# Kernel tuning notes

Measured on AMD Instinct MI355X. Metric: run time of the kernel, lower is better.

The kernel has to match this reference:

```python
import jax, jax.numpy as jnp
import numpy as np

D_MODEL = 1024
NUM_HEADS = 16
D_K = D_MODEL // NUM_HEADS


def setup_inputs() -> dict:
    key = jax.random.key(0)
    ks = jax.random.split(key, 8)
    B, S = 2, 2048
    query = jax.random.normal(ks[0], (B, S, D_MODEL), dtype=jnp.float32)
    k_in = jax.random.normal(ks[1], (B, S, D_MODEL), dtype=jnp.float32)
    value = jax.random.normal(ks[2], (B, S, D_MODEL), dtype=jnp.float32)
    # causal mask: True = masked out (upper triangle above diagonal)
    mask = jnp.triu(jnp.ones((S, S), dtype=bool), k=1)[None, None, :, :]
    scale = 1.0 / np.sqrt(D_MODEL)
    W_q = jax.random.normal(ks[3], (D_MODEL, D_MODEL), dtype=jnp.float32) * scale
    W_k = jax.random.normal(ks[4], (D_MODEL, D_MODEL), dtype=jnp.float32) * scale
    W_v = jax.random.normal(ks[5], (D_MODEL, D_MODEL), dtype=jnp.float32) * scale
    W_o = jax.random.normal(ks[6], (D_MODEL, D_MODEL), dtype=jnp.float32) * scale
    return {"query": query, "key": k_in, "value": value, "mask": mask,
            "W_q": W_q, "W_k": W_k, "W_v": W_v, "W_o": W_o}


def _split(x):
    # [B, S, d_model] -> [B, h, S, d_k]
    B, S, _ = x.shape
    return x.reshape(B, S, NUM_HEADS, D_K).transpose(0, 2, 1, 3)


def reference(query, key, value, mask, W_q, W_k, W_v, W_o):
    # torch nn.Linear(bias=False): y = x @ W.T
    Q = _split(query @ W_q.T)   # [B, h, Sq, d_k]
    K = _split(key @ W_k.T)     # [B, h, Sk, d_k]
    V = _split(value @ W_v.T)   # [B, h, Sk, d_k]
    scores = jnp.einsum('bhqd,bhkd->bhqk', Q, K) / jnp.sqrt(jnp.float32(D_K))
    scores = jnp.where(mask, -jnp.inf, scores)
    attn_w = jax.nn.softmax(scores, axis=-1)
    attn_w = jnp.nan_to_num(attn_w, nan=0.0)
    out = jnp.einsum('bhqk,bhkd->bhqd', attn_w, V)  # [B, h, Sq, d_k]
    B, _, Sq, _ = out.shape
    merged = out.transpose(0, 2, 1, 3).reshape(B, Sq, D_MODEL)
    return merged @ W_o.T
```

## Files before the change

kernel.cpp:

```cpp
#include <hip/hip_runtime.h>
#include <hip/hip_bf16.h>
#include <stdint.h>

typedef __attribute__((ext_vector_type(4))) float f32x4;
typedef __attribute__((ext_vector_type(8))) __bf16 bf16x8;
typedef __attribute__((ext_vector_type(4))) unsigned short us4;

#define SEQ 2048
#define DMODEL 1024
#define NH 16
#define DK 64
#define MTOT 4096

__device__ __forceinline__ unsigned short f2bf(float x) {
  union { float f; unsigned int u; } v; v.f = x;
  unsigned int r = v.u + 0x7fffu + ((v.u >> 16) & 1u);
  return (unsigned short)(r >> 16);
}

__device__ __forceinline__ unsigned int cvtpk(float lo, float hi) {
  unsigned int r;
  asm("v_cvt_pk_bf16_f32 %0, %1, %2" : "=v"(r) : "v"(lo), "v"(hi));
  return r;
}

__device__ __forceinline__ f32x4 mfma_bf16(bf16x8 a, bf16x8 b, f32x4 c) {
  return __builtin_amdgcn_mfma_f32_16x16x32_bf16(a, b, c, 0, 0, 0);
}

__device__ __forceinline__ void gload16(const unsigned short* g, unsigned short* l) {
  __builtin_amdgcn_global_load_lds((__attribute__((address_space(1))) void*)g,
                                   (__attribute__((address_space(3))) void*)l,
                                   16, 0, 0);
}

__global__ void cvt_all(const float* __restrict__ s0, const float* __restrict__ s1,
                        const float* __restrict__ s2, const float* __restrict__ s3,
                        const float* __restrict__ s4, const float* __restrict__ s5,
                        const float* __restrict__ s6,
                        unsigned short* __restrict__ d0, unsigned short* __restrict__ d1,
                        unsigned short* __restrict__ d2, unsigned short* __restrict__ d3,
                        unsigned short* __restrict__ d4, unsigned short* __restrict__ d5,
                        unsigned short* __restrict__ d6) {
  const int y = blockIdx.y;
  const float* s = y == 0 ? s0 : y == 1 ? s1 : y == 2 ? s2 : y == 3 ? s3
                 : y == 4 ? s4 : y == 5 ? s5 : s6;
  unsigned short* d = y == 0 ? d0 : y == 1 ? d1 : y == 2 ? d2 : y == 3 ? d3
                    : y == 4 ? d4 : y == 5 ? d5 : d6;
  const int n4 = (y < 3) ? (MTOT * DMODEL / 4) : (DMODEL * DMODEL / 4);
  const int stride = gridDim.x * blockDim.x;
  for (int i = blockIdx.x * blockDim.x + threadIdx.x; i < n4; i += stride) {
    f32x4 v = reinterpret_cast<const f32x4*>(s)[i];
    us4 o;
    o.x = f2bf(v.x); o.y = f2bf(v.y); o.z = f2bf(v.z); o.w = f2bf(v.w);
    reinterpret_cast<us4*>(d)[i] = o;
  }
}

__global__ __launch_bounds__(256) void gemm_qkv(
    const unsigned short* __restrict__ xq, const unsigned short* __restrict__ xk,
    const unsigned short* __restrict__ xv, const unsigned short* __restrict__ bwq,
    const unsigned short* __restrict__ bwk, const unsigned short* __restrict__ bwv,
    unsigned short* __restrict__ Qh, unsigned short* __restrict__ Kh,
    unsigned short* __restrict__ Vt) {
  const int z = blockIdx.z;
  const unsigned short* A = z == 0 ? xq : (z == 1 ? xk : xv);
  const unsigned short* B = z == 0 ? bwq : (z == 1 ? bwk : bwv);
  unsigned short* out = z == 0 ? Qh : (z == 1 ? Kh : Vt);
  const float scale = z == 0 ? 0.18033688011112042f : 1.0f;

  __shared__ __align__(16) unsigned short lA[128 * 32];
  __shared__ __align__(16) unsigned short lB[128 * 32];
  const int tid = threadIdx.x;
  const int lane = tid & 63;
  const int wid = tid >> 6;
  const int l15 = lane & 15, l4 = lane >> 4;
  const int bm = blockIdx.x, bn = blockIdx.y;
  const int wr = wid >> 1, wc = wid & 1;

  f32x4 acc[4][4] = {};

  const int chunk0 = (wid * 2 + 0) * 64 + lane;
  const int chunk1 = (wid * 2 + 1) * 64 + lane;
  const unsigned short* gA0 = A + (size_t)(bm * 128 + (chunk0 >> 2)) * 1024 + (chunk0 & 3) * 8;
  const unsigned short* gA1 = A + (size_t)(bm * 128 + (chunk1 >> 2)) * 1024 + (chunk1 & 3) * 8;
  const unsigned short* gB0 = B + (size_t)(bn * 128 + (chunk0 >> 2)) * 1024 + (chunk0 & 3) * 8;
  const unsigned short* gB1 = B + (size_t)(bn * 128 + (chunk1 >> 2)) * 1024 + (chunk1 & 3) * 8;
  unsigned short* lA0 = lA + (wid * 2 + 0) * 512;
  unsigned short* lA1 = lA + (wid * 2 + 1) * 512;
  unsigned short* lB0 = lB + (wid * 2 + 0) * 512;
  unsigned short* lB1 = lB + (wid * 2 + 1) * 512;

  for (int kt = 0; kt < 1024; kt += 32) {
    __syncthreads();
    gload16(gA0 + kt, lA0);
    gload16(gA1 + kt, lA1);
    gload16(gB0 + kt, lB0);
    gload16(gB1 + kt, lB1);
    __syncthreads();
    bf16x8 af[4], bfr[4];
#pragma unroll
    for (int i = 0; i < 4; ++i)
      af[i] = *reinterpret_cast<const bf16x8*>(&lA[(wr * 64 + i * 16 + l15) * 32 + l4 * 8]);
#pragma unroll
    for (int j = 0; j < 4; ++j)
      bfr[j] = *reinterpret_cast<const bf16x8*>(&lB[(wc * 64 + j * 16 + l15) * 32 + l4 * 8]);
#pragma unroll
    for (int i = 0; i < 4; ++i)
#pragma unroll
      for (int j = 0; j < 4; ++j)
        acc[i][j] = mfma_bf16(af[i], bfr[j], acc[i][j]);
  }

  const int row0 = bm * 128 + wr * 64;
  const int col0 = bn * 128 + wc * 64;

  if (z < 2) {
#pragma unroll
    for (int i = 0; i < 4; ++i) {
#pragma unroll
      for (int j = 0; j < 4; ++j) {
        const int n = col0 + j * 16 + l15;
        const int h = n >> 6, dd = n & 63;
#pragma unroll
        for (int r = 0; r < 4; ++r) {
          const int m = row0 + i * 16 + l4 * 4 + r;
          const int b = m >> 11, s = m & 2047;
          out[(size_t)(b * NH + h) * (SEQ * DK) + s * DK + dd] = f2bf(acc[i][j][r] * scale);
        }
      }
    }
  } else {
#pragma unroll
    for (int i = 0; i < 4; ++i) {
      const int m0 = row0 + i * 16 + l4 * 4;
      const int b = m0 >> 11, s0 = m0 & 2047;
      const int g = (s0 >> 2) & 7;
      const int col = (s0 & ~31) + ((g & 3) << 3) + ((g >> 2) << 2);
#pragma unroll
      for (int j = 0; j < 4; ++j) {
        const int n = col0 + j * 16 + l15;
        const int h = n >> 6, dd = n & 63;
        us4 pk;
        pk.x = f2bf(acc[i][j][0]);
        pk.y = f2bf(acc[i][j][1]);
        pk.z = f2bf(acc[i][j][2]);
        pk.w = f2bf(acc[i][j][3]);
        *reinterpret_cast<us4*>(&out[(size_t)(b * NH + h) * (DK * SEQ) + dd * SEQ + col]) = pk;
      }
    }
  }
}

__global__ __launch_bounds__(256) void gemm_o(const unsigned short* __restrict__ A,
                                              const unsigned short* __restrict__ B,
                                              float* __restrict__ out) {
  __shared__ __align__(16) unsigned short lA[128 * 32];
  __shared__ __align__(16) unsigned short lB[128 * 32];
  const int tid = threadIdx.x;
  const int lane = tid & 63;
  const int wid = tid >> 6;
  const int l15 = lane & 15, l4 = lane >> 4;
  const int bm = blockIdx.x, bn = blockIdx.y;
  const int wr = wid >> 1, wc = wid & 1;

  f32x4 acc[4][4] = {};

  const int chunk0 = (wid * 2 + 0) * 64 + lane;
  const int chunk1 = (wid * 2 + 1) * 64 + lane;
  const unsigned short* gA0 = A + (size_t)(bm * 128 + (chunk0 >> 2)) * 1024 + (chunk0 & 3) * 8;
  const unsigned short* gA1 = A + (size_t)(bm * 128 + (chunk1 >> 2)) * 1024 + (chunk1 & 3) * 8;
  const unsigned short* gB0 = B + (size_t)(bn * 128 + (chunk0 >> 2)) * 1024 + (chunk0 & 3) * 8;
  const unsigned short* gB1 = B + (size_t)(bn * 128 + (chunk1 >> 2)) * 1024 + (chunk1 & 3) * 8;
  unsigned short* lA0 = lA + (wid * 2 + 0) * 512;
  unsigned short* lA1 = lA + (wid * 2 + 1) * 512;
  unsigned short* lB0 = lB + (wid * 2 + 0) * 512;
  unsigned short* lB1 = lB + (wid * 2 + 1) * 512;

  for (int kt = 0; kt < 1024; kt += 32) {
    __syncthreads();
    gload16(gA0 + kt, lA0);
    gload16(gA1 + kt, lA1);
    gload16(gB0 + kt, lB0);
    gload16(gB1 + kt, lB1);
    __syncthreads();
    bf16x8 af[4], bfr[4];
#pragma unroll
    for (int i = 0; i < 4; ++i)
      af[i] = *reinterpret_cast<const bf16x8*>(&lA[(wr * 64 + i * 16 + l15) * 32 + l4 * 8]);
#pragma unroll
    for (int j = 0; j < 4; ++j)
      bfr[j] = *reinterpret_cast<const bf16x8*>(&lB[(wc * 64 + j * 16 + l15) * 32 + l4 * 8]);
#pragma unroll
    for (int i = 0; i < 4; ++i)
#pragma unroll
      for (int j = 0; j < 4; ++j)
        acc[i][j] = mfma_bf16(af[i], bfr[j], acc[i][j]);
  }

  const int row0 = bm * 128 + wr * 64;
  const int col0 = bn * 128 + wc * 64;
#pragma unroll
  for (int i = 0; i < 4; ++i)
#pragma unroll
    for (int j = 0; j < 4; ++j)
#pragma unroll
      for (int r = 0; r < 4; ++r) {
        const int m = row0 + i * 16 + l4 * 4 + r;
        const int n = col0 + j * 16 + l15;
        out[(size_t)m * DMODEL + n] = acc[i][j][r];
      }
}

__global__ __launch_bounds__(512, 2) void attn_kernel(const unsigned short* __restrict__ Qh,
                                                      const unsigned short* __restrict__ Kh,
                                                      const unsigned short* __restrict__ Vt,
                                                      unsigned short* __restrict__ Mg) {
  __shared__ __align__(16) unsigned short Kl[3][64 * 64];
  __shared__ __align__(16) unsigned short Vl[3][64 * 64];

  const int tid = threadIdx.x;
  const int lane = tid & 63;
  const int w = tid >> 6;
  const int l15 = lane & 15, l4 = lane >> 4;

  const int d = blockIdx.x;
  const int xcd = d & 7;
  const int j = d >> 3;
  const int bh = (j >> 3) * 8 + xcd;
  const int x = j & 7;

  const unsigned short* Qb = Qh + (size_t)bh * SEQ * DK;
  const unsigned short* Kb = Kh + (size_t)bh * SEQ * DK;
  const unsigned short* Vb = Vt + (size_t)bh * DK * SEQ;
  const int bq = bh >> 4, hh = bh & 15;
  unsigned short* Mbase = Mg + (size_t)bq * SEQ * DMODEL + hh * DK;

  const int srow = lane >> 3;
  const int sswz = (lane & 7) ^ srow;
  const unsigned short* KsrcB = Kb + (size_t)(w * 8 + srow) * DK + sswz * 8;
  const unsigned short* VsrcB = Vb + (size_t)(w * 8 + srow) * SEQ + sswz * 8;

  const int l7 = l15 & 7;

  const int taus[2] = {15 - x, x};

#pragma unroll 1
  for (int seg = 0; seg < 2; ++seg) {
    const int tau = taus[seg];
    const int qbase = tau * 128;
    const int q0w = qbase + w * 16;
    const int nt = 2 * tau + 2;

    __syncthreads();

    bf16x8 qf0 = *reinterpret_cast<const bf16x8*>(Qb + (size_t)(q0w + l15) * DK + l4 * 8);
    bf16x8 qf1 = *reinterpret_cast<const bf16x8*>(Qb + (size_t)(q0w + l15) * DK + 32 + l4 * 8);

    f32x4 o[4] = {};
    float mrow = -__builtin_inff();
    float lrow = 0.0f;

    gload16(KsrcB, &Kl[0][w * 512]);
    gload16(VsrcB, &Vl[0][w * 512]);
    gload16(KsrcB + (size_t)64 * DK, &Kl[1][w * 512]);
    gload16(VsrcB + 64, &Vl[1][w * 512]);

    int bi = 0;
#pragma unroll 1
    for (int t = 0; t < nt; ++t) {
      const int kbase = t << 6;
      if (t + 1 < nt) {
        asm volatile("s_waitcnt vmcnt(2)" ::: "memory");
      } else {
        asm volatile("s_waitcnt vmcnt(0)" ::: "memory");
      }
      __builtin_amdgcn_sched_barrier(0);
      __builtin_amdgcn_s_barrier();
      __builtin_amdgcn_sched_barrier(0);

      if (t + 2 < nt) {
        const int pb = (bi == 0) ? 2 : bi - 1;
        gload16(KsrcB + (size_t)(kbase + 128) * DK, &Kl[pb][w * 512]);
        gload16(VsrcB + (kbase + 128), &Vl[pb][w * 512]);
      }

      if (kbase < q0w + 16) {
        const unsigned short* Kc = Kl[bi];
        const unsigned short* Vc = Vl[bi];

        f32x4 sc[4];
        __builtin_amdgcn_s_setprio(1);
#pragma unroll
        for (int c = 0; c < 4; ++c) {
          const int krow = c * 16 + l15;
          bf16x8 kf0 = *reinterpret_cast<const bf16x8*>(&Kc[krow * 64 + ((l4 ^ l7) * 8)]);
          bf16x8 kf1 = *reinterpret_cast<const bf16x8*>(&Kc[krow * 64 + (((4 + l4) ^ l7) * 8)]);
          f32x4 z = {0.f, 0.f, 0.f, 0.f};
          z = mfma_bf16(kf0, qf0, z);
          sc[c] = mfma_bf16(kf1, qf1, z);
        }
        __builtin_amdgcn_s_setprio(0);

        if (kbase + 63 > q0w) {
          const int qg = q0w + l15;
#pragma unroll
          for (int c = 0; c < 4; ++c) {
            const int kp = kbase + c * 16 + l4 * 4;
#pragma unroll
            for (int r = 0; r < 4; ++r)
              if (kp + r > qg) sc[c][r] = -__builtin_inff();
          }
        }

        f32x4 mv = sc[0];
#pragma unroll
        for (int c = 1; c < 4; ++c)
#pragma unroll
          for (int r = 0; r < 4; ++r) mv[r] = fmaxf(mv[r], sc[c][r]);
        float pm = fmaxf(fmaxf(mv[0], mv[1]), fmaxf(mv[2], mv[3]));
        if (!__all(pm - mrow <= 8.0f)) {
          pm = fmaxf(pm, __shfl_xor(pm, 16));
          pm = fmaxf(pm, __shfl_xor(pm, 32));
          const float mn = fmaxf(mrow, pm);
          const float al = __builtin_amdgcn_exp2f(mrow - mn);
          mrow = mn;
          lrow *= al;
#pragma unroll
          for (int dd = 0; dd < 4; ++dd)
#pragma unroll
            for (int r = 0; r < 4; ++r) o[dd][r] *= al;
        }
        union PB { bf16x8 v; unsigned int u[4]; } pbv[2];
        f32x4 sv = {0.f, 0.f, 0.f, 0.f};
#pragma unroll
        for (int c = 0; c < 4; ++c) {
          const float p0 = __builtin_amdgcn_exp2f(sc[c][0] - mrow);
          const float p1 = __builtin_amdgcn_exp2f(sc[c][1] - mrow);
          const float p2 = __builtin_amdgcn_exp2f(sc[c][2] - mrow);
          const float p3 = __builtin_amdgcn_exp2f(sc[c][3] - mrow);
          sv[0] += p0; sv[1] += p1; sv[2] += p2; sv[3] += p3;
          pbv[c >> 1].u[(c & 1) * 2 + 0] = cvtpk(p0, p1);
          pbv[c >> 1].u[(c & 1) * 2 + 1] = cvtpk(p2, p3);
        }
        lrow += (sv[0] + sv[1]) + (sv[2] + sv[3]);

        __builtin_amdgcn_s_setprio(1);
#pragma unroll
        for (int dd = 0; dd < 4; ++dd) {
          const int vrow = dd * 16 + l15;
#pragma unroll
          for (int p = 0; p < 2; ++p) {
            const bf16x8 av = *reinterpret_cast<const bf16x8*>(
                &Vc[vrow * 64 + (((p * 4 + l4) ^ l7) * 8)]);
            o[dd] = mfma_bf16(av, pbv[p].v, o[dd]);
          }
        }
        __builtin_amdgcn_s_setprio(0);
      }

      bi = (bi == 2) ? 0 : bi + 1;
    }

    lrow += __shfl_xor(lrow, 16);
    lrow += __shfl_xor(lrow, 32);
    const float inv = __builtin_amdgcn_rcpf(lrow);
    const int s = q0w + l15;
#pragma unroll
    for (int dd = 0; dd < 4; ++dd) {
      union { us4 h; unsigned int u[2]; } pk;
      pk.u[0] = cvtpk(o[dd][0] * inv, o[dd][1] * inv);
      pk.u[1] = cvtpk(o[dd][2] * inv, o[dd][3] * inv);
      *reinterpret_cast<us4*>(&Mbase[(size_t)s * DMODEL + dd * 16 + l4 * 4]) = pk.h;
    }
  }
}

extern "C" void kernel_launch(void* const* d_in, const int* in_sizes, int n_in,
                              void* d_out, int out_size, void* d_ws, size_t ws_size,
                              hipStream_t stream) {
  (void)in_sizes; (void)n_in; (void)out_size;
  if (ws_size < (size_t)64 * (1 << 20)) return;

  const float* q = (const float*)d_in[0];
  const float* k = (const float*)d_in[1];
  const float* v = (const float*)d_in[2];
  const float* wq = (const float*)d_in[4];
  const float* wk = (const float*)d_in[5];
  const float* wv = (const float*)d_in[6];
  const float* wo = (const float*)d_in[7];

  char* ws = (char*)d_ws;
  unsigned short* xq  = (unsigned short*)(ws + (size_t)0  * (1 << 20));
  unsigned short* xk  = (unsigned short*)(ws + (size_t)8  * (1 << 20));
  unsigned short* xv  = (unsigned short*)(ws + (size_t)16 * (1 << 20));
  unsigned short* bwq = (unsigned short*)(ws + (size_t)24 * (1 << 20));
  unsigned short* bwk = (unsigned short*)(ws + (size_t)26 * (1 << 20));
  unsigned short* bwv = (unsigned short*)(ws + (size_t)28 * (1 << 20));
  unsigned short* bwo = (unsigned short*)(ws + (size_t)30 * (1 << 20));
  unsigned short* Qh  = (unsigned short*)(ws + (size_t)32 * (1 << 20));
  unsigned short* Kh  = (unsigned short*)(ws + (size_t)40 * (1 << 20));
  unsigned short* Vt  = (unsigned short*)(ws + (size_t)48 * (1 << 20));
  unsigned short* Mg  = (unsigned short*)(ws + (size_t)56 * (1 << 20));

  cvt_all<<<dim3(256, 7), 256, 0, stream>>>(q, k, v, wq, wk, wv, wo,
                                            xq, xk, xv, bwq, bwk, bwv, bwo);
  gemm_qkv<<<dim3(32, 8, 3), 256, 0, stream>>>(xq, xk, xv, bwq, bwk, bwv, Qh, Kh, Vt);
  attn_kernel<<<dim3(256), 512, 0, stream>>>(Qh, Kh, Vt, Mg);
  gemm_o<<<dim3(32, 8), 256, 0, stream>>>(Mg, bwo, (float*)d_out);
}
```

Baseline: 135.7 us.

## Fuse activation fp32-to-bf16 conversion into QKV GEMM loads and vectorize epilogues

Removes the separate conversion pass over the three 4096x1024 activation tensors. The QKV GEMMs now load fp32 directly into registers, prefetch the next K tile, convert with packed bf16 instructions and store into LDS. Q/K and O GEMMs swap the MFMA operand order so each lane holds contiguous columns, which allows vectorized epilogue stores. V projection is split into its own kernel. The cost is direct register-staged fp32 loads in place of async global-to-LDS copies for the A operand, with more register pressure.

```diff
diff --git a/kernel.cpp b/kernel.cpp
--- a/kernel.cpp
+++ b/kernel.cpp
@@ -5,6 +5,7 @@
 typedef __attribute__((ext_vector_type(4))) float f32x4;
 typedef __attribute__((ext_vector_type(8))) __bf16 bf16x8;
 typedef __attribute__((ext_vector_type(4))) unsigned short us4;
+typedef __attribute__((ext_vector_type(8))) unsigned short us8;
 
 #define SEQ 2048
 #define DMODEL 1024
@@ -34,20 +35,14 @@
                                    16, 0, 0);
 }
 
-__global__ void cvt_all(const float* __restrict__ s0, const float* __restrict__ s1,
-                        const float* __restrict__ s2, const float* __restrict__ s3,
-                        const float* __restrict__ s4, const float* __restrict__ s5,
-                        const float* __restrict__ s6,
-                        unsigned short* __restrict__ d0, unsigned short* __restrict__ d1,
-                        unsigned short* __restrict__ d2, unsigned short* __restrict__ d3,
-                        unsigned short* __restrict__ d4, unsigned short* __restrict__ d5,
-                        unsigned short* __restrict__ d6) {
+__global__ void cvt_w(const float* __restrict__ s0, const float* __restrict__ s1,
+                      const float* __restrict__ s2, const float* __restrict__ s3,
+                      unsigned short* __restrict__ d0, unsigned short* __restrict__ d1,
+                      unsigned short* __restrict__ d2, unsigned short* __restrict__ d3) {
   const int y = blockIdx.y;
-  const float* s = y == 0 ? s0 : y == 1 ? s1 : y == 2 ? s2 : y == 3 ? s3
-                 : y == 4 ? s4 : y == 5 ? s5 : s6;
-  unsigned short* d = y == 0 ? d0 : y == 1 ? d1 : y == 2 ? d2 : y == 3 ? d3
-                    : y == 4 ? d4 : y == 5 ? d5 : d6;
-  const int n4 = (y < 3) ? (MTOT * DMODEL / 4) : (DMODEL * DMODEL / 4);
+  const float* s = y == 0 ? s0 : y == 1 ? s1 : y == 2 ? s2 : s3;
+  unsigned short* d = y == 0 ? d0 : y == 1 ? d1 : y == 2 ? d2 : d3;
+  const int n4 = DMODEL * DMODEL / 4;
   const int stride = gridDim.x * blockDim.x;
   for (int i = blockIdx.x * blockDim.x + threadIdx.x; i < n4; i += stride) {
     f32x4 v = reinterpret_cast<const f32x4*>(s)[i];
@@ -57,17 +52,15 @@
   }
 }
 
-__global__ __launch_bounds__(256) void gemm_qkv(
-    const unsigned short* __restrict__ xq, const unsigned short* __restrict__ xk,
-    const unsigned short* __restrict__ xv, const unsigned short* __restrict__ bwq,
-    const unsigned short* __restrict__ bwk, const unsigned short* __restrict__ bwv,
-    unsigned short* __restrict__ Qh, unsigned short* __restrict__ Kh,
-    unsigned short* __restrict__ Vt) {
+__global__ __launch_bounds__(256) void gemm_qk(
+    const float* __restrict__ xq, const float* __restrict__ xk,
+    const unsigned short* __restrict__ bwq, const unsigned short* __restrict__ bwk,
+    unsigned short* __restrict__ Qh, unsigned short* __restrict__ Kh) {
   const int z = blockIdx.z;
-  const unsigned short* A = z == 0 ? xq : (z == 1 ? xk : xv);
-  const unsigned short* B = z == 0 ? bwq : (z == 1 ? bwk : bwv);
-  unsigned short* out = z == 0 ? Qh : (z == 1 ? Kh : Vt);
-  const float scale = z == 0 ? 0.18033688011112042f : 1.0f;
+  const float* A = z ? xk : xq;
+  const unsigned short* B = z ? bwk : bwq;
+  unsigned short* out = z ? Kh : Qh;
+  const float scale = z ? 1.0f : 0.18033688011112042f;
 
   __shared__ __align__(16) unsigned short lA[128 * 32];
   __shared__ __align__(16) unsigned short lB[128 * 32];
@@ -82,21 +75,37 @@
 
   const int chunk0 = (wid * 2 + 0) * 64 + lane;
   const int chunk1 = (wid * 2 + 1) * 64 + lane;
-  const unsigned short* gA0 = A + (size_t)(bm * 128 + (chunk0 >> 2)) * 1024 + (chunk0 & 3) * 8;
-  const unsigned short* gA1 = A + (size_t)(bm * 128 + (chunk1 >> 2)) * 1024 + (chunk1 & 3) * 8;
+  const float* gAf0 = A + (size_t)(bm * 128 + (chunk0 >> 2)) * 1024 + (chunk0 & 3) * 8;
+  const float* gAf1 = A + (size_t)(bm * 128 + (chunk1 >> 2)) * 1024 + (chunk1 & 3) * 8;
   const unsigned short* gB0 = B + (size_t)(bn * 128 + (chunk0 >> 2)) * 1024 + (chunk0 & 3) * 8;
   const unsigned short* gB1 = B + (size_t)(bn * 128 + (chunk1 >> 2)) * 1024 + (chunk1 & 3) * 8;
-  unsigned short* lA0 = lA + (wid * 2 + 0) * 512;
-  unsigned short* lA1 = lA + (wid * 2 + 1) * 512;
+  unsigned short* wA0 = lA + chunk0 * 8;
+  unsigned short* wA1 = lA + chunk1 * 8;
   unsigned short* lB0 = lB + (wid * 2 + 0) * 512;
   unsigned short* lB1 = lB + (wid * 2 + 1) * 512;
 
+  f32x4 ra0 = *reinterpret_cast<const f32x4*>(gAf0);
+  f32x4 ra1 = *reinterpret_cast<const f32x4*>(gAf0 + 4);
+  f32x4 rb0 = *reinterpret_cast<const f32x4*>(gAf1);
+  f32x4 rb1 = *reinterpret_cast<const f32x4*>(gAf1 + 4);
+
   for (int kt = 0; kt < 1024; kt += 32) {
     __syncthreads();
-    gload16(gA0 + kt, lA0);
-    gload16(gA1 + kt, lA1);
+    union { us8 h; unsigned int u[4]; } p0, p1;
+    p0.u[0] = cvtpk(ra0.x, ra0.y); p0.u[1] = cvtpk(ra0.z, ra0.w);
+    p0.u[2] = cvtpk(ra1.x, ra1.y); p0.u[3] = cvtpk(ra1.z, ra1.w);
+    p1.u[0] = cvtpk(rb0.x, rb0.y); p1.u[1] = cvtpk(rb0.z, rb0.w);
+    p1.u[2] = cvtpk(rb1.x, rb1.y); p1.u[3] = cvtpk(rb1.z, rb1.w);
+    *reinterpret_cast<us8*>(wA0) = p0.h;
+    *reinterpret_cast<us8*>(wA1) = p1.h;
     gload16(gB0 + kt, lB0);
     gload16(gB1 + kt, lB1);
+    if (kt + 32 < 1024) {
+      ra0 = *reinterpret_cast<const f32x4*>(gAf0 + kt + 32);
+      ra1 = *reinterpret_cast<const f32x4*>(gAf0 + kt + 36);
+      rb0 = *reinterpret_cast<const f32x4*>(gAf1 + kt + 32);
+      rb1 = *reinterpret_cast<const f32x4*>(gAf1 + kt + 36);
+    }
     __syncthreads();
     bf16x8 af[4], bfr[4];
 #pragma unroll
@@ -109,45 +118,105 @@
     for (int i = 0; i < 4; ++i)
 #pragma unroll
       for (int j = 0; j < 4; ++j)
-        acc[i][j] = mfma_bf16(af[i], bfr[j], acc[i][j]);
+        acc[i][j] = mfma_bf16(bfr[j], af[i], acc[i][j]);
   }
 
   const int row0 = bm * 128 + wr * 64;
   const int col0 = bn * 128 + wc * 64;
-
-  if (z < 2) {
-#pragma unroll
-    for (int i = 0; i < 4; ++i) {
-#pragma unroll
-      for (int j = 0; j < 4; ++j) {
-        const int n = col0 + j * 16 + l15;
-        const int h = n >> 6, dd = n & 63;
-#pragma unroll
-        for (int r = 0; r < 4; ++r) {
-          const int m = row0 + i * 16 + l4 * 4 + r;
-          const int b = m >> 11, s = m & 2047;
-          out[(size_t)(b * NH + h) * (SEQ * DK) + s * DK + dd] = f2bf(acc[i][j][r] * scale);
-        }
-      }
-    }
-  } else {
-#pragma unroll
-    for (int i = 0; i < 4; ++i) {
-      const int m0 = row0 + i * 16 + l4 * 4;
-      const int b = m0 >> 11, s0 = m0 & 2047;
-      const int g = (s0 >> 2) & 7;
-      const int col = (s0 & ~31) + ((g & 3) << 3) + ((g >> 2) << 2);
-#pragma unroll
-      for (int j = 0; j < 4; ++j) {
-        const int n = col0 + j * 16 + l15;
-        const int h = n >> 6, dd = n & 63;
-        us4 pk;
-        pk.x = f2bf(acc[i][j][0]);
-        pk.y = f2bf(acc[i][j][1]);
-        pk.z = f2bf(acc[i][j][2]);
-        pk.w = f2bf(acc[i][j][3]);
-        *reinterpret_cast<us4*>(&out[(size_t)(b * NH + h) * (DK * SEQ) + dd * SEQ + col]) = pk;
-      }
+#pragma unroll
+  for (int i = 0; i < 4; ++i) {
+    const int m = row0 + i * 16 + l15;
+    const int b = m >> 11, s = m & 2047;
+#pragma unroll
+    for (int j = 0; j < 4; ++j) {
+      const int n0 = col0 + j * 16 + l4 * 4;
+      const int h = n0 >> 6, dd = n0 & 63;
+      union { us4 h4; unsigned int u[2]; } pk;
+      pk.u[0] = cvtpk(acc[i][j][0] * scale, acc[i][j][1] * scale);
+      pk.u[1] = cvtpk(acc[i][j][2] * scale, acc[i][j][3] * scale);
+      *reinterpret_cast<us4*>(&out[(size_t)(b * NH + h) * (SEQ * DK) + s * DK + dd]) = pk.h4;
+    }
+  }
+}
+
+__global__ __launch_bounds__(256) void gemm_v(
+    const float* __restrict__ xv, const unsigned short* __restrict__ bwv,
+    unsigned short* __restrict__ Vt) {
+  __shared__ __align__(16) unsigned short lA[128 * 32];
+  __shared__ __align__(16) unsigned short lB[128 * 32];
+  const int tid = threadIdx.x;
+  const int lane = tid & 63;
+  const int wid = tid >> 6;
+  const int l15 = lane & 15, l4 = lane >> 4;
+  const int bm = blockIdx.x, bn = blockIdx.y;
+  const int wr = wid >> 1, wc = wid & 1;
+
+  f32x4 acc[4][4] = {};
+
+  const int chunk0 = (wid * 2 + 0) * 64 + lane;
+  const int chunk1 = (wid * 2 + 1) * 64 + lane;
+  const float* gAf0 = xv + (size_t)(bm * 128 + (chunk0 >> 2)) * 1024 + (chunk0 & 3) * 8;
+  const float* gAf1 = xv + (size_t)(bm * 128 + (chunk1 >> 2)) * 1024 + (chunk1 & 3) * 8;
+  const unsigned short* gB0 = bwv + (size_t)(bn * 128 + (chunk0 >> 2)) * 1024 + (chunk0 & 3) * 8;
+  const unsigned short* gB1 = bwv + (size_t)(bn * 128 + (chunk1 >> 2)) * 1024 + (chunk1 & 3) * 8;
+  unsigned short* wA0 = lA + chunk0 * 8;
+  unsigned short* wA1 = lA + chunk1 * 8;
+  unsigned short* lB0 = lB + (wid * 2 + 0) * 512;
+  unsigned short* lB1 = lB + (wid * 2 + 1) * 512;
+
+  f32x4 ra0 = *reinterpret_cast<const f32x4*>(gAf0);
+  f32x4 ra1 = *reinterpret_cast<const f32x4*>(gAf0 + 4);
+  f32x4 rb0 = *reinterpret_cast<const f32x4*>(gAf1);
+  f32x4 rb1 = *reinterpret_cast<const f32x4*>(gAf1 + 4);
+
+  for (int kt = 0; kt < 1024; kt += 32) {
+    __syncthreads();
+    union { us8 h; unsigned int u[4]; } p0, p1;
+    p0.u[0] = cvtpk(ra0.x, ra0.y); p0.u[1] = cvtpk(ra0.z, ra0.w);
+    p0.u[2] = cvtpk(ra1.x, ra1.y); p0.u[3] = cvtpk(ra1.z, ra1.w);
+    p1.u[0] = cvtpk(rb0.x, rb0.y); p1.u[1] = cvtpk(rb0.z, rb0.w);
+    p1.u[2] = cvtpk(rb1.x, rb1.y); p1.u[3] = cvtpk(rb1.z, rb1.w);
+    *reinterpret_cast<us8*>(wA0) = p0.h;
+    *reinterpret_cast<us8*>(wA1) = p1.h;
+    gload16(gB0 + kt, lB0);
+    gload16(gB1 + kt, lB1);
+    if (kt + 32 < 1024) {
+      ra0 = *reinterpret_cast<const f32x4*>(gAf0 + kt + 32);
+      ra1 = *reinterpret_cast<const f32x4*>(gAf0 + kt + 36);
+      rb0 = *reinterpret_cast<const f32x4*>(gAf1 + kt + 32);
+      rb1 = *reinterpret_cast<const f32x4*>(gAf1 + kt + 36);
+    }
+    __syncthreads();
+    bf16x8 af[4], bfr[4];
+#pragma unroll
+    for (int i = 0; i < 4; ++i)
+      af[i] = *reinterpret_cast<const bf16x8*>(&lA[(wr * 64 + i * 16 + l15) * 32 + l4 * 8]);
+#pragma unroll
+    for (int j = 0; j < 4; ++j)
+      bfr[j] = *reinterpret_cast<const bf16x8*>(&lB[(wc * 64 + j * 16 + l15) * 32 + l4 * 8]);
+#pragma unroll
+    for (int i = 0; i < 4; ++i)
+#pragma unroll
+      for (int j = 0; j < 4; ++j)
+        acc[i][j] = mfma_bf16(af[i], bfr[j], acc[i][j]);
+  }
+
+  const int row0 = bm * 128 + wr * 64;
+  const int col0 = bn * 128 + wc * 64;
+#pragma unroll
+  for (int i = 0; i < 4; ++i) {
+    const int m0 = row0 + i * 16 + l4 * 4;
+    const int b = m0 >> 11, s0 = m0 & 2047;
+    const int g = (s0 >> 2) & 7;
+    const int col = (s0 & ~31) + ((g & 3) << 3) + ((g >> 2) << 2);
+#pragma unroll
+    for (int j = 0; j < 4; ++j) {
+      const int n = col0 + j * 16 + l15;
+      const int h = n >> 6, dd = n & 63;
+      union { us4 h4; unsigned int u[2]; } pk;
+      pk.u[0] = cvtpk(acc[i][j][0], acc[i][j][1]);
+      pk.u[1] = cvtpk(acc[i][j][2], acc[i][j][3]);
+      *reinterpret_cast<us4*>(&Vt[(size_t)(b * NH + h) * (DK * SEQ) + dd * SEQ + col]) = pk.h4;
     }
   }
 }
@@ -195,21 +264,20 @@
     for (int i = 0; i < 4; ++i)
 #pragma unroll
       for (int j = 0; j < 4; ++j)
-        acc[i][j] = mfma_bf16(af[i], bfr[j], acc[i][j]);
+        acc[i][j] = mfma_bf16(bfr[j], af[i], acc[i][j]);
   }
 
   const int row0 = bm * 128 + wr * 64;
   const int col0 = bn * 128 + wc * 64;
 #pragma unroll
-  for (int i = 0; i < 4; ++i)
-#pragma unroll
-    for (int j = 0; j < 4; ++j)
-#pragma unroll
-      for (int r = 0; r < 4; ++r) {
-        const int m = row0 + i * 16 + l4 * 4 + r;
-        const int n = col0 + j * 16 + l15;
-        out[(size_t)m * DMODEL + n] = acc[i][j][r];
-      }
+  for (int i = 0; i < 4; ++i) {
+    const int m = row0 + i * 16 + l15;
+#pragma unroll
+    for (int j = 0; j < 4; ++j) {
+      const int n0 = col0 + j * 16 + l4 * 4;
+      *reinterpret_cast<f32x4*>(&out[(size_t)m * DMODEL + n0]) = acc[i][j];
+    }
+  }
 }
 
 __global__ __launch_bounds__(512, 2) void attn_kernel(const unsigned short* __restrict__ Qh,
@@ -391,9 +459,6 @@
   const float* wo = (const float*)d_in[7];
 
   char* ws = (char*)d_ws;
-  unsigned short* xq  = (unsigned short*)(ws + (size_t)0  * (1 << 20));
-  unsigned short* xk  = (unsigned short*)(ws + (size_t)8  * (1 << 20));
-  unsigned short* xv  = (unsigned short*)(ws + (size_t)16 * (1 << 20));
   unsigned short* bwq = (unsigned short*)(ws + (size_t)24 * (1 << 20));
   unsigned short* bwk = (unsigned short*)(ws + (size_t)26 * (1 << 20));
   unsigned short* bwv = (unsigned short*)(ws + (size_t)28 * (1 << 20));
@@ -403,9 +468,9 @@
   unsigned short* Vt  = (unsigned short*)(ws + (size_t)48 * (1 << 20));
   unsigned short* Mg  = (unsigned short*)(ws + (size_t)56 * (1 << 20));
 
-  cvt_all<<<dim3(256, 7), 256, 0, stream>>>(q, k, v, wq, wk, wv, wo,
-                                            xq, xk, xv, bwq, bwk, bwv, bwo);
-  gemm_qkv<<<dim3(32, 8, 3), 256, 0, stream>>>(xq, xk, xv, bwq, bwk, bwv, Qh, Kh, Vt);
+  cvt_w<<<dim3(64, 4), 256, 0, stream>>>(wq, wk, wv, wo, bwq, bwk, bwv, bwo);
+  gemm_qk<<<dim3(32, 8, 2), 256, 0, stream>>>(q, k, bwq, bwk, Qh, Kh);
+  gemm_v<<<dim3(32, 8), 256, 0, stream>>>(v, bwv, Vt);
   attn_kernel<<<dim3(256), 512, 0, stream>>>(Qh, Kh, Vt, Mg);
   gemm_o<<<dim3(32, 8), 256, 0, stream>>>(Mg, bwo, (float*)d_out);
 }
```

Result: no change. 137.2 us (+1.1%).
